# Kernel optimization log

Measured on AMD Instinct MI355X. Metric: run time of the kernel, lower is better.

The kernel has to match this reference:

```python
import jax, jax.numpy as jnp
import numpy as np

SIGMA = 1.0          # from global `args.sigma` in the original repo
ALPHA = 0.99         # self.alpha
TOPK = 4             # torch.topk(W, 4)
NUM_CLASSES = 2
EPS = float(np.finfo(float).eps)


def setup_inputs() -> dict:
    key = jax.random.key(0)
    k1, k2, k3 = jax.random.split(key, 3)
    labeled_inputs = jax.random.normal(k1, (1024, 1024), dtype=jnp.float32)
    labeled_target = jax.random.randint(k2, (1024,), 0, NUM_CLASSES, dtype=jnp.int64)
    unlabeled_inputs = jax.random.normal(k3, (3072, 1024), dtype=jnp.float32)
    return {"labeled_inputs": labeled_inputs,
            "labeled_target": labeled_target,
            "unlabeled_inputs": unlabeled_inputs}


def _label_prop(labeled_inputs, unlabeled_inputs, labeled_target):
    num_support = labeled_inputs.shape[0]
    emb_all = jnp.concatenate([labeled_inputs, unlabeled_inputs], axis=0)  # [N, d]
    N, d = emb_all.shape

    # mean_j (x_i - x_k)_j^2 = (|x_i|^2 + |x_k|^2 - 2 x_i.x_k) / d
    # (algebraically identical to the torch NxNxd broadcast, without materializing it)
    sq = jnp.sum(emb_all * emb_all, axis=1)                 # [N]
    dist = (sq[:, None] + sq[None, :] - 2.0 * (emb_all @ emb_all.T)) / d
    W = jnp.exp(-dist / (2.0 * SIGMA * SIGMA))              # [N, N]

    # zero the diagonal
    eye = jnp.eye(N, dtype=W.dtype)
    W = W * (1.0 - eye)

    # top-k per row -> symmetric binary mask
    _, indices = jax.lax.top_k(W, TOPK)                     # [N, k]
    mask = jnp.zeros_like(W)
    rows = jnp.arange(N)[:, None]
    mask = mask.at[rows, indices].set(1.0)
    mask = ((mask + mask.T) > 0).astype(jnp.float32)
    W = W * mask

    # symmetric degree normalization S = D^{-1/2} W D^{-1/2}
    D = W.sum(axis=0)                                       # [N]
    D_sqrt_inv = jnp.sqrt(1.0 / (D + EPS))
    S = D_sqrt_inv[:, None] * W * D_sqrt_inv[None, :]

    # labels: one-hot support, zeros for queries
    ys = jax.nn.one_hot(labeled_target, NUM_CLASSES, dtype=jnp.float32)
    yu = jnp.zeros((N - num_support, NUM_CLASSES), dtype=jnp.float32)
    y = jnp.concatenate([ys, yu], axis=0)                   # [N, C]

    # F = (I - alpha*S + eps)^{-1} y   (solve == inverse @ y)
    A = jnp.eye(N, dtype=jnp.float32) - ALPHA * S + EPS
    Fk = jnp.linalg.solve(A, y)
    return Fk[num_support:, :]                              # [num_queries, C]


def reference(labeled_inputs, labeled_target, unlabeled_inputs):
    return _label_prop(labeled_inputs, unlabeled_inputs, labeled_target)
```

## Files before the change

kernel.cpp:

```cpp
#include <hip/hip_runtime.h>

#define N_ALL 4096
#define N_LAB 1024
#define DIMF 1024
#define EDGECAP 32768
#define ALPHA_ 0.99f
#define NIT_CH 80
#define EPS_D 2.220446049250313e-16

typedef short bf16x8 __attribute__((ext_vector_type(8)));
typedef float f32x4 __attribute__((ext_vector_type(4)));

struct __align__(8) Edge { unsigned j; float w; };

__device__ inline const float* xrow(const float* L, const float* U, int r) {
  return (r < N_LAB) ? (L + (size_t)r * DIMF) : (U + (size_t)(r - N_LAB) * DIMF);
}

__device__ inline void load_lds16(const void* g, void* l) {
  __builtin_amdgcn_global_load_lds(
      (const __attribute__((address_space(1))) unsigned int*)g,
      (__attribute__((address_space(3))) unsigned int*)l, 16, 0, 0);
}

__device__ inline unsigned short bf16rne(float f) {
  unsigned u = __float_as_uint(f);
  unsigned r = (u + 0x7fffu + ((u >> 16) & 1u)) >> 16;
  return (unsigned short)r;
}

__global__ __launch_bounds__(256) void prep_k(const float* __restrict__ L,
                                              const float* __restrict__ U,
                                              unsigned short* __restrict__ Xbf,
                                              float* __restrict__ sq,
                                              double* __restrict__ sqd) {
  const int row = blockIdx.x;
  const int tid = threadIdx.x;
  const float* src = xrow(L, U, row);
  float4 v = ((const float4*)src)[tid];
  ushort4 h;
  h.x = bf16rne(v.x); h.y = bf16rne(v.y); h.z = bf16rne(v.z); h.w = bf16rne(v.w);
  ((ushort4*)(Xbf + (size_t)row * DIMF))[tid] = h;
  float s = v.x * v.x + v.y * v.y + v.z * v.z + v.w * v.w;
  double sd = (double)v.x * v.x + (double)v.y * v.y +
              (double)v.z * v.z + (double)v.w * v.w;
#pragma unroll
  for (int d = 32; d >= 1; d >>= 1) {
    s += __shfl_xor(s, d);
    sd += __shfl_xor(sd, d);
  }
  __shared__ float wsum[4];
  __shared__ double wsumd[4];
  if ((tid & 63) == 0) { wsum[tid >> 6] = s; wsumd[tid >> 6] = sd; }
  __syncthreads();
  if (tid == 0) {
    sq[row] = wsum[0] + wsum[1] + wsum[2] + wsum[3];
    sqd[row] = wsumd[0] + wsumd[1] + wsumd[2] + wsumd[3];
  }
}

__global__ __launch_bounds__(256) void gemm_w(const unsigned short* __restrict__ Xbf,
                                              const float* __restrict__ sq,
                                              _Float16* __restrict__ Wh) {
  __shared__ unsigned short At[128 * 32];
  __shared__ unsigned short Bt[128 * 32];
  const int tid = threadIdx.x;
  const int wave = tid >> 6, lane = tid & 63;
  const int brow = blockIdx.y * 128, bcol = blockIdx.x * 128;
  const int q = lane >> 4, rl = lane & 15;
  const int wr = (wave >> 1) * 64, wc = (wave & 1) * 64;

  f32x4 acc[4][4] = {};

  const int srow = tid >> 2;
  const int soff = (tid & 3) * 8;

  for (int k0 = 0; k0 < DIMF; k0 += 32) {
#pragma unroll
    for (int half = 0; half < 2; ++half) {
      const unsigned short* ga =
          Xbf + (size_t)(brow + half * 64 + srow) * DIMF + k0 + soff;
      load_lds16(ga, &At[(half * 64 + wave * 16) * 32]);
      const unsigned short* gb =
          Xbf + (size_t)(bcol + half * 64 + srow) * DIMF + k0 + soff;
      load_lds16(gb, &Bt[(half * 64 + wave * 16) * 32]);
    }
    __syncthreads();
    bf16x8 af[4], bf_[4];
#pragma unroll
    for (int t = 0; t < 4; ++t) {
      af[t] = *(const bf16x8*)&At[(wr + t * 16 + rl) * 32 + q * 8];
      bf_[t] = *(const bf16x8*)&Bt[(wc + t * 16 + rl) * 32 + q * 8];
    }
#pragma unroll
    for (int i = 0; i < 4; ++i)
#pragma unroll
      for (int j = 0; j < 4; ++j)
        acc[i][j] = __builtin_amdgcn_mfma_f32_16x16x32_bf16(af[i], bf_[j], acc[i][j], 0, 0, 0);
    __syncthreads();
  }

#pragma unroll
  for (int i = 0; i < 4; ++i) {
#pragma unroll
    for (int j = 0; j < 4; ++j) {
#pragma unroll
      for (int reg = 0; reg < 4; ++reg) {
        int gr = brow + wr + i * 16 + q * 4 + reg;
        int gc = bcol + wc + j * 16 + rl;
        float g = acc[i][j][reg];
        float dist = sq[gr] + sq[gc] - 2.0f * g;
        float val = fmaxf(2600.0f - dist, 0.25f);
        if (gr == gc) val = 0.0f;
        Wh[(size_t)gr * N_ALL + gc] = (_Float16)val;
      }
    }
  }
}

__global__ __launch_bounds__(256) void top8_k(const _Float16* __restrict__ Wh,
                                              unsigned* __restrict__ t8i) {
  const int wave = threadIdx.x >> 6, lane = threadIdx.x & 63;
  const int row = blockIdx.x * 4 + wave;
  const _Float16* Wr = Wh + (size_t)row * N_ALL;
  float bv[8]; unsigned bj[8];
#pragma unroll
  for (int t = 0; t < 8; ++t) { bv[t] = -1.0f; bj[t] = 0xFFFFFFFFu; }
  float minv = -1.0f; int mins = 0;
  for (int s = 0; s < 64; ++s) {
    int j = s * 64 + lane;
    float v = (float)Wr[j];
    if (v > minv) {
#pragma unroll
      for (int t = 0; t < 8; ++t) if (t == mins) { bv[t] = v; bj[t] = (unsigned)j; }
      minv = bv[0]; mins = 0;
#pragma unroll
      for (int t = 1; t < 8; ++t) if (bv[t] < minv) { minv = bv[t]; mins = t; }
    }
  }
  for (int pick = 0; pick < 8; ++pick) {
    unsigned long long best = 0;
#pragma unroll
    for (int t = 0; t < 8; ++t) {
      bool valid = (bv[t] >= 0.0f);
      unsigned long long key =
          ((unsigned long long)__float_as_uint(bv[t]) << 32) |
          (unsigned long long)(0xFFFFFFFFu - bj[t]);
      if (valid && key > best) best = key;
    }
#pragma unroll
    for (int d = 32; d >= 1; d >>= 1) {
      unsigned long long o = __shfl_xor(best, d);
      if (o > best) best = o;
    }
    unsigned wj = 0xFFFFFFFFu - (unsigned)(best & 0xFFFFFFFFull);
    if (lane == 0) t8i[row * 8 + pick] = wj;
#pragma unroll
    for (int t = 0; t < 8; ++t) if (bj[t] == wj) bv[t] = -1.0f;
  }
}

__global__ __launch_bounds__(256) void rerank_k(const float* __restrict__ L,
                                                const float* __restrict__ U,
                                                const double* __restrict__ sqd,
                                                const unsigned* __restrict__ t8i,
                                                unsigned* __restrict__ t4i) {
  const int wave = threadIdx.x >> 6, lane = threadIdx.x & 63;
  const int row = blockIdx.x * 4 + wave;
  const float* xi = xrow(L, U, row);
  float xr[16];
#pragma unroll
  for (int t = 0; t < 16; ++t) xr[t] = xi[t * 64 + lane];
  unsigned cj[8];
  double cw[8];
#pragma unroll
  for (int c = 0; c < 8; ++c) cj[c] = t8i[row * 8 + c];
  for (int c = 0; c < 8; ++c) {
    const float* xj = xrow(L, U, (int)cj[c]);
    double s = 0.0;
#pragma unroll
    for (int t = 0; t < 16; ++t) s += (double)xr[t] * xj[t * 64 + lane];
#pragma unroll
    for (int d = 32; d >= 1; d >>= 1) s += __shfl_xor(s, d);
    double dist = (sqd[row] + sqd[cj[c]] - 2.0 * s) * (1.0 / 1024.0);
    cw[c] = exp(-0.5 * dist);
  }
  if (lane == 0) {
#pragma unroll
    for (int pick = 0; pick < 4; ++pick) {
      int ms = -1;
      double mv = -1.0;
      unsigned mj = 0xFFFFFFFFu;
#pragma unroll
      for (int c = 0; c < 8; ++c) {
        bool better = (cw[c] > mv) || (cw[c] == mv && cj[c] < mj);
        if (cw[c] >= 0.0 && better) { mv = cw[c]; mj = cj[c]; ms = c; }
      }
      t4i[row * 4 + pick] = mj;
      cw[ms] = -2.0;
    }
  }
}

__global__ __launch_bounds__(256) void cnt4_k(const unsigned* __restrict__ t4i,
                                              unsigned* __restrict__ nn) {
  const int wave = threadIdx.x >> 6, lane = threadIdx.x & 63;
  const int i = blockIdx.x * 4 + wave;
  const uint4 mine = ((const uint4*)t4i)[i];
  unsigned base = 0;
  for (int j0 = 0; j0 < N_ALL; j0 += 64) {
    int j = j0 + lane;
    uint4 tj = ((const uint4*)t4i)[j];
    bool keep = (mine.x == (unsigned)j) | (mine.y == (unsigned)j) |
                (mine.z == (unsigned)j) | (mine.w == (unsigned)j) |
                (tj.x == (unsigned)i) | (tj.y == (unsigned)i) |
                (tj.z == (unsigned)i) | (tj.w == (unsigned)i);
    keep = keep && (j != i);
    base += (unsigned)__popcll(__ballot(keep));
  }
  if (lane == 0) nn[i] = base;
}

__global__ __launch_bounds__(64) void scanP_k(const unsigned* __restrict__ nn,
                                              unsigned* __restrict__ rowPtr,
                                              const int* __restrict__ lab,
                                              int* __restrict__ labflag) {
  const int lane = threadIdx.x;
  const long long* l64 = (const long long*)lab;
  int bad = 0;
#pragma unroll
  for (int k = 0; k < 8; ++k) {
    long long v = l64[k * 64 + lane];
    if (v != 0 && v != 1) bad = 1;
  }
  unsigned long long bm = __ballot(bad);
  if (lane == 0) labflag[0] = (bm != 0ull) ? 0 : 1;
  unsigned running = 0;
  for (int j0 = 0; j0 < N_ALL; j0 += 64) {
    int v = (int)nn[j0 + lane];
    int incl = v;
#pragma unroll
    for (int d = 1; d < 64; d <<= 1) {
      int t = __shfl_up(incl, d);
      if (lane >= d) incl += t;
    }
    rowPtr[j0 + lane] = running + (unsigned)(incl - v);
    running += (unsigned)__shfl(incl, 63);
  }
  if (lane == 0) rowPtr[N_ALL] = running;
}

__global__ __launch_bounds__(256) void csrfill_k(const unsigned* __restrict__ t4i,
                                                 const unsigned* __restrict__ rowPtr,
                                                 Edge* __restrict__ edges,
                                                 unsigned* __restrict__ eRow) {
  const int wave = threadIdx.x >> 6, lane = threadIdx.x & 63;
  const int i = blockIdx.x * 4 + wave;
  const uint4 mine = ((const uint4*)t4i)[i];
  unsigned base = rowPtr[i];
  for (int j0 = 0; j0 < N_ALL; j0 += 64) {
    int j = j0 + lane;
    uint4 tj = ((const uint4*)t4i)[j];
    bool keep = (mine.x == (unsigned)j) | (mine.y == (unsigned)j) |
                (mine.z == (unsigned)j) | (mine.w == (unsigned)j) |
                (tj.x == (unsigned)i) | (tj.y == (unsigned)i) |
                (tj.z == (unsigned)i) | (tj.w == (unsigned)i);
    keep = keep && (j != i);
    unsigned long long m = __ballot(keep);
    if (keep) {
      unsigned pos = base + (unsigned)__popcll(m & ((1ull << lane) - 1ull));
      edges[pos].j = (unsigned)j;
      edges[pos].w = 0.0f;
      eRow[pos] = (unsigned)i;
    }
    base += (unsigned)__popcll(m);
  }
}

__global__ __launch_bounds__(256) void edgeval_k(const float* __restrict__ L,
                                                 const float* __restrict__ U,
                                                 const double* __restrict__ sqd,
                                                 const unsigned* __restrict__ rowPtr,
                                                 const unsigned* __restrict__ eRow,
                                                 Edge* __restrict__ edges) {
  const int wave = threadIdx.x >> 6, lane = threadIdx.x & 63;
  const unsigned e = blockIdx.x * 4 + wave;
  if (e >= rowPtr[N_ALL]) return;
  const unsigned i = eRow[e];
  const unsigned j = edges[e].j;
  const float* xi = xrow(L, U, (int)i);
  const float* xj = xrow(L, U, (int)j);
  double s = 0.0;
#pragma unroll
  for (int t = 0; t < 16; ++t)
    s += (double)xi[t * 64 + lane] * xj[t * 64 + lane];
#pragma unroll
  for (int d = 32; d >= 1; d >>= 1) s += __shfl_xor(s, d);
  if (lane == 0) {
    double dist = (sqd[i] + sqd[j] - 2.0 * s) * (1.0 / 1024.0);
    edges[e].w = (float)exp(-0.5 * dist);
  }
}

__global__ __launch_bounds__(256) void degE_k(const unsigned* __restrict__ rowPtr,
                                              const Edge* __restrict__ edges,
                                              float* __restrict__ Dis) {
  const int wave = threadIdx.x >> 6, lane = threadIdx.x & 63;
  const int i = blockIdx.x * 4 + wave;
  const unsigned b0 = rowPtr[i], b1 = rowPtr[i + 1];
  double ds = 0.0;
  for (unsigned e = b0 + lane; e < b1; e += 64) ds += (double)edges[e].w;
#pragma unroll
  for (int d = 32; d >= 1; d >>= 1) ds += __shfl_xor(ds, d);
  if (lane == 0) Dis[i] = (float)sqrt(1.0 / (ds + EPS_D));
}

__global__ __launch_bounds__(256) void scaleE_k(const unsigned* __restrict__ rowPtr,
                                                const unsigned* __restrict__ eRow,
                                                const float* __restrict__ Dis,
                                                Edge* __restrict__ edges) {
  const unsigned e = blockIdx.x * 256 + threadIdx.x;
  if (e >= rowPtr[N_ALL]) return;
  Edge ed = edges[e];
  edges[e].w = ed.w * Dis[eRow[e]] * Dis[ed.j];
}

__global__ __launch_bounds__(256) void init_k(const int* __restrict__ lab,
                                              const int* __restrict__ labflag,
                                              float2* __restrict__ x,
                                              float2* __restrict__ r,
                                              float2* __restrict__ d) {
  const int m = blockIdx.x * 256 + threadIdx.x;
  const int isI64 = labflag[0];
  float2 b = make_float2(0.0f, 0.0f);
  if (m < N_LAB) {
    int c = isI64 ? lab[2 * m] : lab[m];
    b.x = (c == 0) ? 1.0f : 0.0f;
    b.y = (c == 1) ? 1.0f : 0.0f;
  }
  x[m] = make_float2(0.0f, 0.0f);
  r[m] = b;
  d[m] = b;
}

__global__ __launch_bounds__(512) void chebit_k(const Edge* __restrict__ edges,
                                                const unsigned* __restrict__ rowPtr,
                                                const float2* __restrict__ dIn,
                                                float2* __restrict__ dOut,
                                                float2* __restrict__ x,
                                                float2* __restrict__ r,
                                                float c1, float c2, int last) {
  const int row = blockIdx.x * 8 + (threadIdx.x >> 6);
  const int lane = threadIdx.x & 63;
  const unsigned b0 = rowPtr[row], b1 = rowPtr[row + 1];
  float ax = 0.0f, ay = 0.0f;
  for (unsigned e = b0 + lane; e < b1; e += 64) {
    Edge ed = edges[e];
    float2 dj = dIn[ed.j];
    ax += ed.w * dj.x;
    ay += ed.w * dj.y;
  }
#pragma unroll
  for (int d = 32; d >= 1; d >>= 1) {
    ax += __shfl_xor(ax, d);
    ay += __shfl_xor(ay, d);
  }
  if (lane == 0) {
    float2 di = dIn[row], xi = x[row], ri = r[row];
    xi.x += di.x; xi.y += di.y;
    ri.x += ALPHA_ * ax - di.x;
    ri.y += ALPHA_ * ay - di.y;
    x[row] = xi;
    r[row] = ri;
    if (!last) {
      float2 dn;
      dn.x = c1 * di.x + c2 * ri.x;
      dn.y = c1 * di.y + c2 * ri.y;
      dOut[row] = dn;
    }
  }
}

__global__ __launch_bounds__(256) void out_k(const float2* __restrict__ x,
                                             float2* __restrict__ out) {
  const int q = blockIdx.x * 256 + threadIdx.x;
  out[q] = x[N_LAB + q];
}

extern "C" void kernel_launch(void* const* d_in, const int* in_sizes, int n_in,
                              void* d_out, int out_size, void* d_ws, size_t ws_size,
                              hipStream_t stream) {
  int iL = 0, iT = 1, iU = 2;
  for (int i = 0; i < n_in; ++i) {
    if (in_sizes[i] == N_LAB * DIMF) iL = i;
    else if (in_sizes[i] == (N_ALL - N_LAB) * DIMF) iU = i;
    else iT = i;
  }
  const float* L = (const float*)d_in[iL];
  const int* lab = (const int*)d_in[iT];
  const float* U = (const float*)d_in[iU];
  float2* out = (float2*)d_out;

  char* w = (char*)d_ws;
  size_t off = 0;
  auto alloc = [&](size_t bytes) {
    void* p = (void*)(w + off);
    off += (bytes + 255) & ~(size_t)255;
    return p;
  };
  _Float16* Wh = (_Float16*)alloc((size_t)N_ALL * N_ALL * 2);
  unsigned short* Xbf = (unsigned short*)alloc((size_t)N_ALL * DIMF * 2);
  float* sq = (float*)alloc(N_ALL * 4);
  double* sqd = (double*)alloc(N_ALL * 8);
  unsigned* t8i = (unsigned*)alloc(N_ALL * 8 * 4);
  unsigned* t4i = (unsigned*)alloc(N_ALL * 4 * 4);
  float* Dis = (float*)alloc(N_ALL * 4);
  unsigned* nn = (unsigned*)alloc(N_ALL * 4);
  unsigned* rowPtr = (unsigned*)alloc((N_ALL + 1) * 4);
  int* labflag = (int*)alloc(256);
  Edge* edges = (Edge*)alloc((size_t)EDGECAP * sizeof(Edge));
  unsigned* eRow = (unsigned*)alloc((size_t)EDGECAP * 4);
  float2* xv = (float2*)alloc(N_ALL * 8);
  float2* rv = (float2*)alloc(N_ALL * 8);
  float2* dv0 = (float2*)alloc(N_ALL * 8);
  float2* dv1 = (float2*)alloc(N_ALL * 8);
  if (off > ws_size) return;

  prep_k<<<N_ALL, 256, 0, stream>>>(L, U, Xbf, sq, sqd);
  gemm_w<<<dim3(32, 32), 256, 0, stream>>>(Xbf, sq, Wh);
  top8_k<<<N_ALL / 4, 256, 0, stream>>>(Wh, t8i);
  rerank_k<<<N_ALL / 4, 256, 0, stream>>>(L, U, sqd, t8i, t4i);
  cnt4_k<<<N_ALL / 4, 256, 0, stream>>>(t4i, nn);
  scanP_k<<<1, 64, 0, stream>>>(nn, rowPtr, lab, labflag);
  csrfill_k<<<N_ALL / 4, 256, 0, stream>>>(t4i, rowPtr, edges, eRow);
  edgeval_k<<<EDGECAP / 4, 256, 0, stream>>>(L, U, sqd, rowPtr, eRow, edges);
  degE_k<<<N_ALL / 4, 256, 0, stream>>>(rowPtr, edges, Dis);
  scaleE_k<<<EDGECAP / 256, 256, 0, stream>>>(rowPtr, eRow, Dis, edges);
  init_k<<<N_ALL / 256, 256, 0, stream>>>(lab, labflag, xv, rv, dv0);

  const double theta = 1.0, delta = 0.992;
  const double sigma1 = theta / delta;
  double rho = delta / theta;
  float2* dA = dv0;
  float2* dB = dv1;
  for (int k = 0; k < NIT_CH; ++k) {
    const int last = (k == NIT_CH - 1);
    const double rho_new = 1.0 / (2.0 * sigma1 - rho);
    const float c1 = (float)(rho_new * rho);
    const float c2 = (float)(2.0 * rho_new / delta);
    chebit_k<<<N_ALL / 8, 512, 0, stream>>>(edges, rowPtr, dA, dB, xv, rv,
                                            c1, c2, last);
    rho = rho_new;
    float2* t = dA; dA = dB; dB = t;
  }
  out_k<<<(N_ALL - N_LAB) / 256, 256, 0, stream>>>(xv, out);
}
```

Measured before the change: 559.5 us.

## Exploit symmetry in similarity GEMM and fuse init/output into Chebyshev iterations

The similarity GEMM now computes only upper-triangular tiles, writes the tile and writes its transpose through an LDS staging buffer to fill the mirrored block. This roughly halves the MFMA work and operand loads. Separately, the initialization kernel is folded into the first Chebyshev iteration, which computes the one-hot label vector inline, and the output copy is folded into the last iteration. This removes two launches. The cost is extra LDS per GEMM block, which may reduce occupancy, plus additional branching in the iteration kernel.

```diff
diff --git a/kernel.cpp b/kernel.cpp
--- a/kernel.cpp
+++ b/kernel.cpp
@@ -62,11 +62,14 @@
 __global__ __launch_bounds__(256) void gemm_w(const unsigned short* __restrict__ Xbf,
                                               const float* __restrict__ sq,
                                               _Float16* __restrict__ Wh) {
+  if (blockIdx.x < blockIdx.y) return;
   __shared__ unsigned short At[128 * 32];
   __shared__ unsigned short Bt[128 * 32];
+  __shared__ _Float16 Tt[128 * 136];
   const int tid = threadIdx.x;
   const int wave = tid >> 6, lane = tid & 63;
   const int brow = blockIdx.y * 128, bcol = blockIdx.x * 128;
+  const int offdiag = (blockIdx.x != blockIdx.y);
   const int q = lane >> 4, rl = lane & 15;
   const int wr = (wave >> 1) * 64, wc = (wave & 1) * 64;
 
@@ -106,15 +109,28 @@
     for (int j = 0; j < 4; ++j) {
 #pragma unroll
       for (int reg = 0; reg < 4; ++reg) {
-        int gr = brow + wr + i * 16 + q * 4 + reg;
-        int gc = bcol + wc + j * 16 + rl;
+        const int lr = wr + i * 16 + q * 4 + reg;
+        const int lc = wc + j * 16 + rl;
+        const int gr = brow + lr;
+        const int gc = bcol + lc;
         float g = acc[i][j][reg];
         float dist = sq[gr] + sq[gc] - 2.0f * g;
         float val = fmaxf(2600.0f - dist, 0.25f);
         if (gr == gc) val = 0.0f;
         Wh[(size_t)gr * N_ALL + gc] = (_Float16)val;
+        Tt[lc * 136 + lr] = (_Float16)val;
       }
     }
+  }
+  if (offdiag) {
+    __syncthreads();
+    const int r = tid >> 1;
+    const int h = tid & 1;
+    _Float16* dst = Wh + (size_t)(bcol + r) * N_ALL + brow + h * 64;
+    const _Float16* srcT = Tt + r * 136 + h * 64;
+#pragma unroll
+    for (int k2 = 0; k2 < 8; ++k2)
+      *(uint4*)&dst[k2 * 8] = *(const uint4*)&srcT[k2 * 8];
   }
 }
 
@@ -325,40 +341,41 @@
   edges[e].w = ed.w * Dis[eRow[e]] * Dis[ed.j];
 }
 
-__global__ __launch_bounds__(256) void init_k(const int* __restrict__ lab,
-                                              const int* __restrict__ labflag,
-                                              float2* __restrict__ x,
-                                              float2* __restrict__ r,
-                                              float2* __restrict__ d) {
-  const int m = blockIdx.x * 256 + threadIdx.x;
-  const int isI64 = labflag[0];
-  float2 b = make_float2(0.0f, 0.0f);
-  if (m < N_LAB) {
-    int c = isI64 ? lab[2 * m] : lab[m];
-    b.x = (c == 0) ? 1.0f : 0.0f;
-    b.y = (c == 1) ? 1.0f : 0.0f;
-  }
-  x[m] = make_float2(0.0f, 0.0f);
-  r[m] = b;
-  d[m] = b;
-}
-
 __global__ __launch_bounds__(512) void chebit_k(const Edge* __restrict__ edges,
                                                 const unsigned* __restrict__ rowPtr,
                                                 const float2* __restrict__ dIn,
                                                 float2* __restrict__ dOut,
                                                 float2* __restrict__ x,
                                                 float2* __restrict__ r,
-                                                float c1, float c2, int last) {
+                                                const int* __restrict__ lab,
+                                                const int* __restrict__ labflag,
+                                                float2* __restrict__ out,
+                                                float c1, float c2,
+                                                int first, int last) {
   const int row = blockIdx.x * 8 + (threadIdx.x >> 6);
   const int lane = threadIdx.x & 63;
   const unsigned b0 = rowPtr[row], b1 = rowPtr[row + 1];
   float ax = 0.0f, ay = 0.0f;
-  for (unsigned e = b0 + lane; e < b1; e += 64) {
-    Edge ed = edges[e];
-    float2 dj = dIn[ed.j];
-    ax += ed.w * dj.x;
-    ay += ed.w * dj.y;
+  if (first) {
+    const int isI64 = labflag[0];
+    for (unsigned e = b0 + lane; e < b1; e += 64) {
+      Edge ed = edges[e];
+      float2 dj = make_float2(0.0f, 0.0f);
+      if (ed.j < (unsigned)N_LAB) {
+        int c = isI64 ? lab[2 * ed.j] : lab[ed.j];
+        dj.x = (c == 0) ? 1.0f : 0.0f;
+        dj.y = (c == 1) ? 1.0f : 0.0f;
+      }
+      ax += ed.w * dj.x;
+      ay += ed.w * dj.y;
+    }
+  } else {
+    for (unsigned e = b0 + lane; e < b1; e += 64) {
+      Edge ed = edges[e];
+      float2 dj = dIn[ed.j];
+      ax += ed.w * dj.x;
+      ay += ed.w * dj.y;
+    }
   }
 #pragma unroll
   for (int d = 32; d >= 1; d >>= 1) {
@@ -366,7 +383,22 @@
     ay += __shfl_xor(ay, d);
   }
   if (lane == 0) {
-    float2 di = dIn[row], xi = x[row], ri = r[row];
+    float2 di, xi, ri;
+    if (first) {
+      float2 b = make_float2(0.0f, 0.0f);
+      if (row < N_LAB) {
+        int c = labflag[0] ? lab[2 * row] : lab[row];
+        b.x = (c == 0) ? 1.0f : 0.0f;
+        b.y = (c == 1) ? 1.0f : 0.0f;
+      }
+      di = b;
+      xi = make_float2(0.0f, 0.0f);
+      ri = b;
+    } else {
+      di = dIn[row];
+      xi = x[row];
+      ri = r[row];
+    }
     xi.x += di.x; xi.y += di.y;
     ri.x += ALPHA_ * ax - di.x;
     ri.y += ALPHA_ * ay - di.y;
@@ -377,14 +409,10 @@
       dn.x = c1 * di.x + c2 * ri.x;
       dn.y = c1 * di.y + c2 * ri.y;
       dOut[row] = dn;
-    }
-  }
-}
-
-__global__ __launch_bounds__(256) void out_k(const float2* __restrict__ x,
-                                             float2* __restrict__ out) {
-  const int q = blockIdx.x * 256 + threadIdx.x;
-  out[q] = x[N_LAB + q];
+    } else if (row >= N_LAB) {
+      out[row - N_LAB] = xi;
+    }
+  }
 }
 
 extern "C" void kernel_launch(void* const* d_in, const int* in_sizes, int n_in,
@@ -436,7 +464,6 @@
   edgeval_k<<<EDGECAP / 4, 256, 0, stream>>>(L, U, sqd, rowPtr, eRow, edges);
   degE_k<<<N_ALL / 4, 256, 0, stream>>>(rowPtr, edges, Dis);
   scaleE_k<<<EDGECAP / 256, 256, 0, stream>>>(rowPtr, eRow, Dis, edges);
-  init_k<<<N_ALL / 256, 256, 0, stream>>>(lab, labflag, xv, rv, dv0);
 
   const double theta = 1.0, delta = 0.992;
   const double sigma1 = theta / delta;
@@ -444,14 +471,15 @@
   float2* dA = dv0;
   float2* dB = dv1;
   for (int k = 0; k < NIT_CH; ++k) {
+    const int first = (k == 0);
     const int last = (k == NIT_CH - 1);
     const double rho_new = 1.0 / (2.0 * sigma1 - rho);
     const float c1 = (float)(rho_new * rho);
     const float c2 = (float)(2.0 * rho_new / delta);
     chebit_k<<<N_ALL / 8, 512, 0, stream>>>(edges, rowPtr, dA, dB, xv, rv,
-                                            c1, c2, last);
+                                            lab, labflag, out, c1, c2,
+                                            first, last);
     rho = rho_new;
     float2* t = dA; dA = dB; dB = t;
   }
-  out_k<<<(N_ALL - N_LAB) / 256, 256, 0, stream>>>(xv, out);
-}
+}
```

New measurement: 584.6 us. 4.5% more time.
